# Performance work log

Measured on AMD Instinct MI355X. Metric: run time of the kernel, lower is better.

Reference implementation:

```python
import jax, jax.numpy as jnp
import numpy as np

H = 64   # hidden_dim
E = 5    # num_edge_features
F = 6    # num_node_features
B, W, N = 8, 12, 200
LN_EPS = 1e-5


def _lstm_layer(x, Wih, Whh, bih, bhh):
    # x: [BN, W, Fin] -> full output sequence [BN, W, H] (PyTorch gate order i,f,g,o)
    BN = x.shape[0]
    h0 = jnp.zeros((BN, Whh.shape[1]), x.dtype)
    def step(carry, xt):
        h, c = carry
        g = xt @ Wih.T + h @ Whh.T + (bih + bhh)
        i, f, gg, o = jnp.split(g, 4, axis=-1)
        c = jax.nn.sigmoid(f) * c + jax.nn.sigmoid(i) * jnp.tanh(gg)
        h = jax.nn.sigmoid(o) * jnp.tanh(c)
        return (h, c), h
    _, ys = jax.lax.scan(step, (h0, h0), jnp.swapaxes(x, 0, 1))
    return jnp.swapaxes(ys, 0, 1)


def _layernorm(x, g, b):
    mu = jnp.mean(x, axis=-1, keepdims=True)
    var = jnp.mean(jnp.square(x - mu), axis=-1, keepdims=True)
    return (x - mu) * jax.lax.rsqrt(var + LN_EPS) * g + b


def setup_inputs() -> dict:
    key = jax.random.key(0)
    ks = jax.random.split(key, 32)
    s = 0.05
    d = {
        'node_features': jax.random.normal(ks[0], (B, W, N, F), jnp.float32),
        'edge_features': jax.random.normal(ks[1], (B, W, N, N, E), jnp.float32),
        'adjacency': jax.random.uniform(ks[2], (B, N, N), jnp.float32),
        # LSTM layer 0 (input F) and layer 1 (input H)
        'Wih0': jax.random.normal(ks[3], (4 * H, F), jnp.float32) * s,
        'Whh0': jax.random.normal(ks[4], (4 * H, H), jnp.float32) * s,
        'bih0': jax.random.normal(ks[5], (4 * H,), jnp.float32) * s,
        'bhh0': jax.random.normal(ks[6], (4 * H,), jnp.float32) * s,
        'Wih1': jax.random.normal(ks[7], (4 * H, H), jnp.float32) * s,
        'Whh1': jax.random.normal(ks[8], (4 * H, H), jnp.float32) * s,
        'bih1': jax.random.normal(ks[9], (4 * H,), jnp.float32) * s,
        'bhh1': jax.random.normal(ks[10], (4 * H,), jnp.float32) * s,
        # 2 GCN layers: linear, edge projection, layernorm
        'gcn_W': jax.random.normal(ks[11], (2, H, H), jnp.float32) * s,
        'gcn_b': jax.random.normal(ks[12], (2, H), jnp.float32) * s,
        'ep_W': jax.random.normal(ks[13], (2, H, E), jnp.float32) * s,
        'ep_b': jax.random.normal(ks[14], (2, H), jnp.float32) * s,
        'ln_g': jnp.ones((2, H), jnp.float32),
        'ln_b': jnp.zeros((2, H), jnp.float32),
        # edge MLP: (2H+E) -> H -> H//2 -> 1
        'mlp_W1': jax.random.normal(ks[15], (H, 2 * H + E), jnp.float32) * s,
        'mlp_b1': jax.random.normal(ks[16], (H,), jnp.float32) * s,
        'mlp_W2': jax.random.normal(ks[17], (H // 2, H), jnp.float32) * s,
        'mlp_b2': jax.random.normal(ks[18], (H // 2,), jnp.float32) * s,
        'mlp_W3': jax.random.normal(ks[19], (1, H // 2), jnp.float32) * s,
        'mlp_b3': jax.random.normal(ks[20], (1,), jnp.float32) * s,
    }
    return d


def reference(node_features, edge_features, adjacency,
              Wih0, Whh0, bih0, bhh0, Wih1, Whh1, bih1, bhh1,
              gcn_W, gcn_b, ep_W, ep_b, ln_g, ln_b,
              mlp_W1, mlp_b1, mlp_W2, mlp_b2, mlp_W3, mlp_b3):
    Bn, Wn, Nn, _ = node_features.shape
    # [B,W,N,F] -> [B*N, W, F]
    x = jnp.transpose(node_features, (0, 2, 1, 3)).reshape(Bn * Nn, Wn, -1)
    y0 = _lstm_layer(x, Wih0, Whh0, bih0, bhh0)      # dropout between layers: eval mode (identity)
    y1 = _lstm_layer(y0, Wih1, Whh1, bih1, bhh1)
    h = y1[:, -1, :].reshape(Bn, Nn, H)

    edge_last = edge_features[:, -1]                 # [B,N,N,E]
    for i in range(2):
        edge_h = edge_last @ ep_W[i].T + ep_b[i]     # [B,N,N,H]
        messages = jnp.einsum('bij,bijn->bin', adjacency, edge_h)
        updated = h @ gcn_W[i].T + gcn_b[i] + messages
        h = jax.nn.relu(_layernorm(updated, ln_g[i], ln_b[i]))
        # dropout: eval mode (identity)

    h_i = jnp.broadcast_to(h[:, :, None, :], (Bn, Nn, Nn, H))
    h_j = jnp.broadcast_to(h[:, None, :, :], (Bn, Nn, Nn, H))
    edge_input = jnp.concatenate([h_i, h_j, edge_last], axis=-1)  # [B,N,N,2H+E]
    z = jax.nn.relu(edge_input @ mlp_W1.T + mlp_b1)
    z = jax.nn.relu(z @ mlp_W2.T + mlp_b2)
    logits = (z @ mlp_W3.T + mlp_b3)[..., 0]
    return jax.nn.sigmoid(logits)
```

## Files before the change

kernel.cpp:

```cpp
#include <hip/hip_runtime.h>
#include <math.h>


#define Hd   64
#define Ed   5
#define Fd   6
#define Bd   8
#define Wd   12
#define Nd   200
#define NSEQ (Bd*Nd)
#define NG   (4*Hd)
#define SEQPB 8
#define LNEPS 1e-5f

__device__ __forceinline__ float sigm(float x) { return 1.0f / (1.0f + __expf(-x)); }
__device__ __forceinline__ float tanh_fast(float x) {
  float ax = fabsf(x);
  float t  = __expf(-2.0f * ax);
  float r  = (1.0f - t) / (1.0f + t);
  return copysignf(r, x);
}

__global__ __launch_bounds__(256) void k_prep(
    const float* __restrict__ gcn_W, const float* __restrict__ ep_W,
    const float* __restrict__ W1,
    float* __restrict__ gcnWT, float* __restrict__ epWT,
    float* __restrict__ W1aT, float* __restrict__ W1bT)
{
  int idx = blockIdx.x * 256 + threadIdx.x;
  if (idx < 8192) {
    int round = idx >> 12, rem = idx & 4095;
    int k = rem >> 6, u = rem & 63;
    gcnWT[idx] = gcn_W[round * 4096 + u * 64 + k];
  } else if (idx < 8832) {
    int r0 = idx - 8192;
    int round = r0 / 320, rem = r0 % 320;
    int e = rem >> 6, u = rem & 63;
    epWT[r0] = ep_W[round * 320 + u * Ed + e];
  } else if (idx < 12928) {
    int r0 = idx - 8832;
    int k = r0 >> 6, n = r0 & 63;
    W1aT[r0] = W1[n * 133 + k];
  } else if (idx < 17024) {
    int r0 = idx - 12928;
    int k = r0 >> 6, n = r0 & 63;
    W1bT[r0] = W1[n * 133 + 64 + k];
  }
}

__global__ __launch_bounds__(512, 2) void k_lstm_fused(
    const float* __restrict__ nf,
    const float* __restrict__ Wih0, const float* __restrict__ Whh0,
    const float* __restrict__ bih0, const float* __restrict__ bhh0,
    const float* __restrict__ Wih1, const float* __restrict__ Whh1,
    const float* __restrict__ bih1, const float* __restrict__ bhh1,
    float* __restrict__ hout)
{
  __shared__ float x_sh[SEQPB][Wd * Fd];
  __shared__ float h0_sh[SEQPB][Hd];
  __shared__ float h1_sh[SEQPB][Hd];
  __shared__ float g0_sh[SEQPB][NG];
  __shared__ float g1_sh[SEQPB][NG];

  const int tid  = threadIdx.x;
  const int seq0 = blockIdx.x * SEQPB;
  const int b    = seq0 / Nd;
  const int n0   = seq0 % Nd;

  for (int idx = tid; idx < SEQPB * Wd * Fd; idx += 512) {
    int s = idx / (Wd * Fd), r = idx - s * (Wd * Fd);
    int t = r / Fd, f = r - t * Fd;
    x_sh[s][r] = nf[((b * Wd + t) * Nd + (n0 + s)) * Fd + f];
  }
  ((float*)h0_sh)[tid >= 512 ? 0 : tid] = 0.f;
  ((float*)h1_sh)[tid >= 512 ? 0 : tid] = 0.f;

  const bool isL0 = (tid < 256);
  const int j  = tid & 255;
  const int jt = j >> 6;
  const int u  = tid & 63;
  const int w  = (tid >> 6) & 3;

  float4 wh[16];
  float4 wi1[16];
  float  wx[Fd];
  float  bias;
  if (isL0) {
    const float4* wr = (const float4*)(Whh0 + j * Hd);
    #pragma unroll
    for (int q = 0; q < 16; ++q) wh[q] = wr[q];
    #pragma unroll
    for (int f = 0; f < Fd; ++f) wx[f] = Wih0[j * Fd + f];
    bias = bih0[j] + bhh0[j];
  } else {
    const float4* wr = (const float4*)(Whh1 + j * Hd);
    #pragma unroll
    for (int q = 0; q < 16; ++q) wh[q] = wr[q];
    const float4* xr = (const float4*)(Wih1 + j * Hd);
    #pragma unroll
    for (int q = 0; q < 16; ++q) wi1[q] = xr[q];
    bias = bih1[j] + bhh1[j];
  }

  float cA = 0.f, cB = 0.f;
  float hA = 0.f, hB = 0.f;
  __syncthreads();

  for (int t = 0; t <= Wd; ++t) {
    if (isL0) {
      if (t < Wd) {
        #pragma unroll 2
        for (int s = 0; s < SEQPB; ++s) {
          const float* xp = &x_sh[s][t * Fd];
          float a0 = bias, a1 = 0.f, a2 = 0.f, a3 = 0.f;
          #pragma unroll
          for (int f = 0; f < Fd; ++f) a1 += xp[f] * wx[f];
          const float4* h4 = (const float4*)h0_sh[s];
          #pragma unroll
          for (int q = 0; q < 16; ++q) {
            float4 hv = h4[q];
            float d = hv.x * wh[q].x + hv.y * wh[q].y + hv.z * wh[q].z + hv.w * wh[q].w;
            if ((q & 3) == 0) a0 += d; else if ((q & 3) == 1) a1 += d;
            else if ((q & 3) == 2) a2 += d; else a3 += d;
          }
          float acc = (a0 + a1) + (a2 + a3);
          g0_sh[s][j] = (jt == 2) ? tanh_fast(acc) : sigm(acc);
        }
      }
    } else {
      if (t >= 1) {
        #pragma unroll 2
        for (int s = 0; s < SEQPB; ++s) {
          const float4* y4 = (const float4*)h0_sh[s];
          float xacc = 0.f;
          #pragma unroll
          for (int q = 0; q < 16; ++q) {
            float4 yv = y4[q];
            xacc = fmaf(yv.x, wi1[q].x, xacc);
            xacc = fmaf(yv.y, wi1[q].y, xacc);
            xacc = fmaf(yv.z, wi1[q].z, xacc);
            xacc = fmaf(yv.w, wi1[q].w, xacc);
          }
          xacc += bias;
          float a0 = xacc, a1 = 0.f, a2 = 0.f, a3 = 0.f;
          const float4* h4 = (const float4*)h1_sh[s];
          #pragma unroll
          for (int q = 0; q < 16; ++q) {
            float4 hv = h4[q];
            float d = hv.x * wh[q].x + hv.y * wh[q].y + hv.z * wh[q].z + hv.w * wh[q].w;
            if ((q & 3) == 0) a0 += d; else if ((q & 3) == 1) a1 += d;
            else if ((q & 3) == 2) a2 += d; else a3 += d;
          }
          float acc = (a0 + a1) + (a2 + a3);
          g1_sh[s][j] = (jt == 2) ? tanh_fast(acc) : sigm(acc);
        }
      }
    }
    __syncthreads();

    if (isL0) {
      if (t < Wd) {
        const float* gb = g0_sh[w];
        float iv = gb[u], fv = gb[64 + u], gv = gb[128 + u], ov = gb[192 + u];
        cA = fv * cA + iv * gv;
        hA = ov * tanh_fast(cA);
        h0_sh[w][u] = hA;
        const float* gb2 = g0_sh[w + 4];
        float iv2 = gb2[u], fv2 = gb2[64 + u], gv2 = gb2[128 + u], ov2 = gb2[192 + u];
        cB = fv2 * cB + iv2 * gv2;
        hB = ov2 * tanh_fast(cB);
        h0_sh[w + 4][u] = hB;
      }
    } else {
      if (t >= 1) {
        const float* gb = g1_sh[w];
        float iv = gb[u], fv = gb[64 + u], gv = gb[128 + u], ov = gb[192 + u];
        cA = fv * cA + iv * gv;
        hA = ov * tanh_fast(cA);
        h1_sh[w][u] = hA;
        const float* gb2 = g1_sh[w + 4];
        float iv2 = gb2[u], fv2 = gb2[64 + u], gv2 = gb2[128 + u], ov2 = gb2[192 + u];
        cB = fv2 * cB + iv2 * gv2;
        hB = ov2 * tanh_fast(cB);
        h1_sh[w + 4][u] = hB;
      }
    }
    __syncthreads();
  }

  if (!isL0) {
    hout[(seq0 + w) * Hd + u]     = hA;
    hout[(seq0 + w + 4) * Hd + u] = hB;
  }
}

__global__ __launch_bounds__(256) void k_node(
    const float* __restrict__ ef,    const float* __restrict__ adj,
    const float* __restrict__ h0,
    const float* __restrict__ gcnWT, const float* __restrict__ gcn_b,
    const float* __restrict__ epWT,  const float* __restrict__ ep_b,
    const float* __restrict__ ln_g,  const float* __restrict__ ln_b,
    const float* __restrict__ W1aT,  const float* __restrict__ W1bT,
    const float* __restrict__ b1,
    float* __restrict__ uu, float* __restrict__ vt)
{
  __shared__ float ef_sh[Nd * Ed];
  __shared__ float adj_sh[Nd];
  __shared__ float red[4][6];
  __shared__ float w6[6];
  __shared__ float hcur[Hd];

  const int row = blockIdx.x;
  const int b = row / Nd, i = row % Nd;
  const int tid = threadIdx.x;

  const float* efrow = ef + (size_t)(((b * Wd + (Wd - 1)) * Nd + i)) * (Nd * Ed);
  for (int idx = tid; idx < Nd * Ed; idx += 256) ef_sh[idx] = efrow[idx];
  const float* adjrow = adj + (b * Nd + i) * Nd;
  if (tid < Nd) adj_sh[tid] = adjrow[tid];
  if (tid < Hd) hcur[tid] = h0[row * Hd + tid];
  __syncthreads();

  float p[6] = {0.f, 0.f, 0.f, 0.f, 0.f, 0.f};
  if (tid < Nd) {
    float a = adj_sh[tid];
    p[5] = a;
    #pragma unroll
    for (int k = 0; k < Ed; ++k) p[k] = a * ef_sh[tid * Ed + k];
  }
  #pragma unroll
  for (int k = 0; k < 6; ++k) {
    float v = p[k];
    for (int off = 32; off > 0; off >>= 1) v += __shfl_down(v, off);
    p[k] = v;
  }
  if ((tid & 63) == 0) {
    #pragma unroll
    for (int k = 0; k < 6; ++k) red[tid >> 6][k] = p[k];
  }
  __syncthreads();
  if (tid < 6)
    w6[tid] = red[0][tid] + red[1][tid] + red[2][tid] + red[3][tid];
  __syncthreads();

  const int u = tid & 63;
  #pragma unroll
  for (int round = 0; round < 2; ++round) {
    float hnew = 0.f;
    if (tid < 64) {
      const float* gwT = gcnWT + round * 4096;
      const float* ewT = epWT  + round * 320;
      float acc = gcn_b[round * Hd + u] + w6[5] * ep_b[round * Hd + u];
      #pragma unroll
      for (int e = 0; e < Ed; ++e) acc += w6[e] * ewT[e * 64 + u];
      #pragma unroll 8
      for (int k = 0; k < Hd; ++k) acc += hcur[k] * gwT[k * 64 + u];

      float mu = acc;
      #pragma unroll
      for (int off = 1; off < 64; off <<= 1) mu += __shfl_xor(mu, off);
      mu *= (1.f / 64.f);
      float d = acc - mu;
      float var = d * d;
      #pragma unroll
      for (int off = 1; off < 64; off <<= 1) var += __shfl_xor(var, off);
      var *= (1.f / 64.f);
      float v = d * rsqrtf(var + LNEPS) * ln_g[round * Hd + u] + ln_b[round * Hd + u];
      hnew = fmaxf(v, 0.f);
    }
    __syncthreads();
    if (tid < 64) hcur[tid] = hnew;
    __syncthreads();
  }

  if (tid < 64) {
    float acc = b1[tid];
    #pragma unroll 8
    for (int k = 0; k < Hd; ++k) acc += hcur[k] * W1aT[k * 64 + tid];
    uu[row * Hd + tid] = acc;
  } else if (tid < 128) {
    const int n = tid - 64;
    float acc = 0.f;
    #pragma unroll 8
    for (int k = 0; k < Hd; ++k) acc += hcur[k] * W1bT[k * 64 + n];
    vt[n * NSEQ + row] = acc;
  }
}

__global__ __launch_bounds__(256) void k_mlp(
    const float* __restrict__ ef,
    const float* __restrict__ u, const float* __restrict__ vt,
    const float* __restrict__ W1,
    const float* __restrict__ W2, const float* __restrict__ b2,
    const float* __restrict__ W3, const float* __restrict__ b3,
    float* __restrict__ out)
{
  const int idx = blockIdx.x * 256 + threadIdx.x;
  const int b   = idx / (Nd * Nd);
  const int rem = idx - b * Nd * Nd;
  const int i   = rem / Nd;
  const int jj  = rem - i * Nd;

  const float* e = ef + (((b * Wd + (Wd - 1)) * Nd + i) * Nd + jj) * Ed;
  float e5[Ed];
  #pragma unroll
  for (int q = 0; q < Ed; ++q) e5[q] = e[q];

  const float* ur = u + (b * Nd + i) * Hd;
  const int vcol = b * Nd + jj;

  float z1[64];
  #pragma unroll
  for (int k = 0; k < 64; ++k) {
    float acc = ur[k] + vt[k * NSEQ + vcol];
    const float* w1c = W1 + k * 133 + 128;
    #pragma unroll
    for (int q = 0; q < Ed; ++q) acc += e5[q] * w1c[q];
    z1[k] = fmaxf(acc, 0.f);
  }

  float logit = b3[0];
  #pragma unroll 4
  for (int o = 0; o < 32; ++o) {
    float a0 = b2[o], a1 = 0.f, a2 = 0.f, a3 = 0.f;
    const float* w2 = W2 + o * 64;
    #pragma unroll
    for (int k = 0; k < 64; k += 4) {
      a0 += w2[k]     * z1[k];
      a1 += w2[k + 1] * z1[k + 1];
      a2 += w2[k + 2] * z1[k + 2];
      a3 += w2[k + 3] * z1[k + 3];
    }
    float z2 = fmaxf((a0 + a1) + (a2 + a3), 0.f);
    logit += W3[o] * z2;
  }
  out[idx] = 1.f / (1.f + __expf(-logit));
}

extern "C" void kernel_launch(void* const* d_in, const int* in_sizes, int n_in,
                              void* d_out, int out_size, void* d_ws, size_t ws_size,
                              hipStream_t stream) {
  (void)in_sizes; (void)n_in; (void)out_size; (void)ws_size;
  const float* nf   = (const float*)d_in[0];
  const float* ef   = (const float*)d_in[1];
  const float* adj  = (const float*)d_in[2];
  const float* Wih0 = (const float*)d_in[3];
  const float* Whh0 = (const float*)d_in[4];
  const float* bih0 = (const float*)d_in[5];
  const float* bhh0 = (const float*)d_in[6];
  const float* Wih1 = (const float*)d_in[7];
  const float* Whh1 = (const float*)d_in[8];
  const float* bih1 = (const float*)d_in[9];
  const float* bhh1 = (const float*)d_in[10];
  const float* gcnW = (const float*)d_in[11];
  const float* gcnB = (const float*)d_in[12];
  const float* epW  = (const float*)d_in[13];
  const float* epB  = (const float*)d_in[14];
  const float* lnG  = (const float*)d_in[15];
  const float* lnB  = (const float*)d_in[16];
  const float* W1   = (const float*)d_in[17];
  const float* b1   = (const float*)d_in[18];
  const float* W2   = (const float*)d_in[19];
  const float* b2   = (const float*)d_in[20];
  const float* W3   = (const float*)d_in[21];
  const float* b3   = (const float*)d_in[22];
  float* out = (float*)d_out;

  float* ws   = (float*)d_ws;
  float* h0   = ws;
  float* uu   = h0   + 102400;
  float* vt   = uu   + 102400;
  float* gWT  = vt   + 102400;
  float* eWT  = gWT  + 8192;
  float* W1aT = eWT  + 640;
  float* W1bT = W1aT + 4096;

  k_prep      <<<67,        256, 0, stream>>>(gcnW, epW, W1, gWT, eWT, W1aT, W1bT);
  k_lstm_fused<<<NSEQ/SEQPB,512, 0, stream>>>(nf, Wih0, Whh0, bih0, bhh0,
                                              Wih1, Whh1, bih1, bhh1, h0);
  k_node      <<<1600,      256, 0, stream>>>(ef, adj, h0, gWT, gcnB, eWT, epB,
                                              lnG, lnB, W1aT, W1bT, b1, uu, vt);
  k_mlp       <<<1250,      256, 0, stream>>>(ef, uu, vt, W1, W2, b2, W3, b3, out);
}
```

Before: 266.0 us.

## Keep LSTM hidden state in registers, broadcast via readlane, pipeline layer-1 input projection

Each warp now keeps its hidden and cell state for all 8 sequences in registers, and the h·W products read h values through readlane broadcasts instead of shared memory. The layer-1 input projection moves to the layer-0 half of the block so it runs one step ahead, and the gate buffers are double-buffered, which removes the second __syncthreads per step. The cost is that every warp redundantly computes the state update for all sequences, the per-thread register load grows (wi1 plus wh on the same threads, arrays of 8), and the occupancy hint of 2 blocks per SM is dropped.

```diff
diff --git a/kernel.cpp b/kernel.cpp
--- a/kernel.cpp
+++ b/kernel.cpp
@@ -19,6 +19,9 @@
   float t  = __expf(-2.0f * ax);
   float r  = (1.0f - t) / (1.0f + t);
   return copysignf(r, x);
+}
+__device__ __forceinline__ float rdl(float v, int l) {
+  return __int_as_float(__builtin_amdgcn_readlane(__float_as_int(v), l));
 }
 
 __global__ __launch_bounds__(256) void k_prep(
@@ -48,7 +51,7 @@
   }
 }
 
-__global__ __launch_bounds__(512, 2) void k_lstm_fused(
+__global__ __launch_bounds__(512) void k_lstm_fused(
     const float* __restrict__ nf,
     const float* __restrict__ Wih0, const float* __restrict__ Whh0,
     const float* __restrict__ bih0, const float* __restrict__ bhh0,
@@ -57,10 +60,9 @@
     float* __restrict__ hout)
 {
   __shared__ float x_sh[SEQPB][Wd * Fd];
-  __shared__ float h0_sh[SEQPB][Hd];
-  __shared__ float h1_sh[SEQPB][Hd];
-  __shared__ float g0_sh[SEQPB][NG];
-  __shared__ float g1_sh[SEQPB][NG];
+  __shared__ float g0_sh[2][SEQPB][NG];
+  __shared__ float g1_sh[2][SEQPB][NG];
+  __shared__ float x1_sh[2][SEQPB][NG];
 
   const int tid  = threadIdx.x;
   const int seq0 = blockIdx.x * SEQPB;
@@ -72,125 +74,136 @@
     int t = r / Fd, f = r - t * Fd;
     x_sh[s][r] = nf[((b * Wd + t) * Nd + (n0 + s)) * Fd + f];
   }
-  ((float*)h0_sh)[tid >= 512 ? 0 : tid] = 0.f;
-  ((float*)h1_sh)[tid >= 512 ? 0 : tid] = 0.f;
-
-  const bool isL0 = (tid < 256);
-  const int j  = tid & 255;
-  const int jt = j >> 6;
-  const int u  = tid & 63;
-  const int w  = (tid >> 6) & 3;
+
+  const bool isA = (tid < 256);
+  const int j    = tid & 255;
+  const int jt   = j >> 6;
+  const int lane = tid & 63;
 
   float4 wh[16];
   float4 wi1[16];
   float  wx[Fd];
-  float  bias;
-  if (isL0) {
+  float  bias0 = 0.f, bias1 = 0.f;
+  if (isA) {
     const float4* wr = (const float4*)(Whh0 + j * Hd);
     #pragma unroll
     for (int q = 0; q < 16; ++q) wh[q] = wr[q];
     #pragma unroll
     for (int f = 0; f < Fd; ++f) wx[f] = Wih0[j * Fd + f];
-    bias = bih0[j] + bhh0[j];
+    bias0 = bih0[j] + bhh0[j];
+    const float4* xr = (const float4*)(Wih1 + j * Hd);
+    #pragma unroll
+    for (int q = 0; q < 16; ++q) wi1[q] = xr[q];
+    bias1 = bih1[j] + bhh1[j];
   } else {
     const float4* wr = (const float4*)(Whh1 + j * Hd);
     #pragma unroll
     for (int q = 0; q < 16; ++q) wh[q] = wr[q];
-    const float4* xr = (const float4*)(Wih1 + j * Hd);
-    #pragma unroll
-    for (int q = 0; q < 16; ++q) wi1[q] = xr[q];
-    bias = bih1[j] + bhh1[j];
-  }
-
-  float cA = 0.f, cB = 0.f;
-  float hA = 0.f, hB = 0.f;
+  }
+
+  float hr[SEQPB], cr[SEQPB];
+  #pragma unroll
+  for (int s = 0; s < SEQPB; ++s) { hr[s] = 0.f; cr[s] = 0.f; }
   __syncthreads();
 
-  for (int t = 0; t <= Wd; ++t) {
-    if (isL0) {
+  for (int t = 0; t <= Wd + 1; ++t) {
+    if (isA) {
       if (t < Wd) {
-        #pragma unroll 2
+        #pragma unroll
         for (int s = 0; s < SEQPB; ++s) {
           const float* xp = &x_sh[s][t * Fd];
-          float a0 = bias, a1 = 0.f, a2 = 0.f, a3 = 0.f;
+          float a0 = bias0, a1 = 0.f, a2 = 0.f, a3 = 0.f;
           #pragma unroll
           for (int f = 0; f < Fd; ++f) a1 += xp[f] * wx[f];
-          const float4* h4 = (const float4*)h0_sh[s];
+          float xacc = 0.f;
           #pragma unroll
           for (int q = 0; q < 16; ++q) {
-            float4 hv = h4[q];
-            float d = hv.x * wh[q].x + hv.y * wh[q].y + hv.z * wh[q].z + hv.w * wh[q].w;
+            float hx = rdl(hr[s], 4 * q + 0);
+            float hy = rdl(hr[s], 4 * q + 1);
+            float hz = rdl(hr[s], 4 * q + 2);
+            float hw = rdl(hr[s], 4 * q + 3);
+            float d = hx * wh[q].x + hy * wh[q].y + hz * wh[q].z + hw * wh[q].w;
+            if ((q & 3) == 0) a0 += d; else if ((q & 3) == 1) a1 += d;
+            else if ((q & 3) == 2) a2 += d; else a3 += d;
+            xacc = fmaf(hx, wi1[q].x, xacc);
+            xacc = fmaf(hy, wi1[q].y, xacc);
+            xacc = fmaf(hz, wi1[q].z, xacc);
+            xacc = fmaf(hw, wi1[q].w, xacc);
+          }
+          float acc = (a0 + a1) + (a2 + a3);
+          g0_sh[t & 1][s][j] = (jt == 2) ? tanh_fast(acc) : sigm(acc);
+          if (t >= 1) x1_sh[t & 1][s][j] = xacc + bias1;
+        }
+      } else if (t == Wd) {
+        #pragma unroll
+        for (int s = 0; s < SEQPB; ++s) {
+          float xacc = 0.f;
+          #pragma unroll
+          for (int q = 0; q < 16; ++q) {
+            float hx = rdl(hr[s], 4 * q + 0);
+            float hy = rdl(hr[s], 4 * q + 1);
+            float hz = rdl(hr[s], 4 * q + 2);
+            float hw = rdl(hr[s], 4 * q + 3);
+            xacc = fmaf(hx, wi1[q].x, xacc);
+            xacc = fmaf(hy, wi1[q].y, xacc);
+            xacc = fmaf(hz, wi1[q].z, xacc);
+            xacc = fmaf(hw, wi1[q].w, xacc);
+          }
+          x1_sh[t & 1][s][j] = xacc + bias1;
+        }
+      }
+    } else {
+      if (t >= 2) {
+        #pragma unroll
+        for (int s = 0; s < SEQPB; ++s) {
+          float a0 = x1_sh[(t - 1) & 1][s][j];
+          float a1 = 0.f, a2 = 0.f, a3 = 0.f;
+          #pragma unroll
+          for (int q = 0; q < 16; ++q) {
+            float hx = rdl(hr[s], 4 * q + 0);
+            float hy = rdl(hr[s], 4 * q + 1);
+            float hz = rdl(hr[s], 4 * q + 2);
+            float hw = rdl(hr[s], 4 * q + 3);
+            float d = hx * wh[q].x + hy * wh[q].y + hz * wh[q].z + hw * wh[q].w;
             if ((q & 3) == 0) a0 += d; else if ((q & 3) == 1) a1 += d;
             else if ((q & 3) == 2) a2 += d; else a3 += d;
           }
           float acc = (a0 + a1) + (a2 + a3);
-          g0_sh[s][j] = (jt == 2) ? tanh_fast(acc) : sigm(acc);
-        }
-      }
-    } else {
-      if (t >= 1) {
-        #pragma unroll 2
-        for (int s = 0; s < SEQPB; ++s) {
-          const float4* y4 = (const float4*)h0_sh[s];
-          float xacc = 0.f;
-          #pragma unroll
-          for (int q = 0; q < 16; ++q) {
-            float4 yv = y4[q];
-            xacc = fmaf(yv.x, wi1[q].x, xacc);
-            xacc = fmaf(yv.y, wi1[q].y, xacc);
-            xacc = fmaf(yv.z, wi1[q].z, xacc);
-            xacc = fmaf(yv.w, wi1[q].w, xacc);
-          }
-          xacc += bias;
-          float a0 = xacc, a1 = 0.f, a2 = 0.f, a3 = 0.f;
-          const float4* h4 = (const float4*)h1_sh[s];
-          #pragma unroll
-          for (int q = 0; q < 16; ++q) {
-            float4 hv = h4[q];
-            float d = hv.x * wh[q].x + hv.y * wh[q].y + hv.z * wh[q].z + hv.w * wh[q].w;
-            if ((q & 3) == 0) a0 += d; else if ((q & 3) == 1) a1 += d;
-            else if ((q & 3) == 2) a2 += d; else a3 += d;
-          }
-          float acc = (a0 + a1) + (a2 + a3);
-          g1_sh[s][j] = (jt == 2) ? tanh_fast(acc) : sigm(acc);
+          g1_sh[t & 1][s][j] = (jt == 2) ? tanh_fast(acc) : sigm(acc);
         }
       }
     }
     __syncthreads();
 
-    if (isL0) {
+    if (isA) {
       if (t < Wd) {
-        const float* gb = g0_sh[w];
-        float iv = gb[u], fv = gb[64 + u], gv = gb[128 + u], ov = gb[192 + u];
-        cA = fv * cA + iv * gv;
-        hA = ov * tanh_fast(cA);
-        h0_sh[w][u] = hA;
-        const float* gb2 = g0_sh[w + 4];
-        float iv2 = gb2[u], fv2 = gb2[64 + u], gv2 = gb2[128 + u], ov2 = gb2[192 + u];
-        cB = fv2 * cB + iv2 * gv2;
-        hB = ov2 * tanh_fast(cB);
-        h0_sh[w + 4][u] = hB;
+        #pragma unroll
+        for (int s = 0; s < SEQPB; ++s) {
+          const float* gb = g0_sh[t & 1][s];
+          float iv = gb[lane], fv = gb[64 + lane];
+          float gv = gb[128 + lane], ov = gb[192 + lane];
+          cr[s] = fv * cr[s] + iv * gv;
+          hr[s] = ov * tanh_fast(cr[s]);
+        }
       }
     } else {
-      if (t >= 1) {
-        const float* gb = g1_sh[w];
-        float iv = gb[u], fv = gb[64 + u], gv = gb[128 + u], ov = gb[192 + u];
-        cA = fv * cA + iv * gv;
-        hA = ov * tanh_fast(cA);
-        h1_sh[w][u] = hA;
-        const float* gb2 = g1_sh[w + 4];
-        float iv2 = gb2[u], fv2 = gb2[64 + u], gv2 = gb2[128 + u], ov2 = gb2[192 + u];
-        cB = fv2 * cB + iv2 * gv2;
-        hB = ov2 * tanh_fast(cB);
-        h1_sh[w + 4][u] = hB;
+      if (t >= 2) {
+        #pragma unroll
+        for (int s = 0; s < SEQPB; ++s) {
+          const float* gb = g1_sh[t & 1][s];
+          float iv = gb[lane], fv = gb[64 + lane];
+          float gv = gb[128 + lane], ov = gb[192 + lane];
+          cr[s] = fv * cr[s] + iv * gv;
+          hr[s] = ov * tanh_fast(cr[s]);
+        }
       }
     }
-    __syncthreads();
-  }
-
-  if (!isL0) {
-    hout[(seq0 + w) * Hd + u]     = hA;
-    hout[(seq0 + w + 4) * Hd + u] = hB;
+  }
+
+  if (tid >= 256 && tid < 320) {
+    #pragma unroll
+    for (int s = 0; s < SEQPB; ++s)
+      hout[(seq0 + s) * Hd + lane] = hr[s];
   }
 }
 
```

New measurement: 275.4 us. 1.04x slower.

## Rebalance LSTM layer work, use readlane GCN in node kernel, batch MLP loads

Applied to the files above, without the earlier changes.

The layer-1 input projection (Wih1·h0) moves to the layer-0 threads, which compute it alongside their recurrent dot product and pass it through a double-buffered shared array, so the layer-1 half only does its own recurrence. This adds one pipeline step. The node kernel keeps the hidden vector in registers, broadcasts it with readlane instead of shared memory, and drops two barriers. The MLP kernel groups its u/vt loads in blocks of eight to expose memory-level parallelism. Layer-0 threads now hold more registers, which risks spills at 512 threads per block.

```diff
diff --git a/kernel.cpp b/kernel.cpp
--- a/kernel.cpp
+++ b/kernel.cpp
@@ -19,6 +19,9 @@
   float t  = __expf(-2.0f * ax);
   float r  = (1.0f - t) / (1.0f + t);
   return copysignf(r, x);
+}
+__device__ __forceinline__ float rdl(float v, int l) {
+  return __int_as_float(__builtin_amdgcn_readlane(__float_as_int(v), l));
 }
 
 __global__ __launch_bounds__(256) void k_prep(
@@ -61,6 +64,7 @@
   __shared__ float h1_sh[SEQPB][Hd];
   __shared__ float g0_sh[SEQPB][NG];
   __shared__ float g1_sh[SEQPB][NG];
+  __shared__ float x1_sh[2][SEQPB][NG];
 
   const int tid  = threadIdx.x;
   const int seq0 = blockIdx.x * SEQPB;
@@ -72,10 +76,10 @@
     int t = r / Fd, f = r - t * Fd;
     x_sh[s][r] = nf[((b * Wd + t) * Nd + (n0 + s)) * Fd + f];
   }
-  ((float*)h0_sh)[tid >= 512 ? 0 : tid] = 0.f;
-  ((float*)h1_sh)[tid >= 512 ? 0 : tid] = 0.f;
-
-  const bool isL0 = (tid < 256);
+  ((float*)h0_sh)[tid] = 0.f;
+  ((float*)h1_sh)[tid] = 0.f;
+
+  const bool isA = (tid < 256);
   const int j  = tid & 255;
   const int jt = j >> 6;
   const int u  = tid & 63;
@@ -84,37 +88,38 @@
   float4 wh[16];
   float4 wi1[16];
   float  wx[Fd];
-  float  bias;
-  if (isL0) {
+  float  bias0 = 0.f, bias1 = 0.f;
+  if (isA) {
     const float4* wr = (const float4*)(Whh0 + j * Hd);
     #pragma unroll
     for (int q = 0; q < 16; ++q) wh[q] = wr[q];
     #pragma unroll
     for (int f = 0; f < Fd; ++f) wx[f] = Wih0[j * Fd + f];
-    bias = bih0[j] + bhh0[j];
+    bias0 = bih0[j] + bhh0[j];
+    const float4* xr = (const float4*)(Wih1 + j * Hd);
+    #pragma unroll
+    for (int q = 0; q < 16; ++q) wi1[q] = xr[q];
+    bias1 = bih1[j] + bhh1[j];
   } else {
     const float4* wr = (const float4*)(Whh1 + j * Hd);
     #pragma unroll
     for (int q = 0; q < 16; ++q) wh[q] = wr[q];
-    const float4* xr = (const float4*)(Wih1 + j * Hd);
-    #pragma unroll
-    for (int q = 0; q < 16; ++q) wi1[q] = xr[q];
-    bias = bih1[j] + bhh1[j];
   }
 
   float cA = 0.f, cB = 0.f;
   float hA = 0.f, hB = 0.f;
   __syncthreads();
 
-  for (int t = 0; t <= Wd; ++t) {
-    if (isL0) {
+  for (int t = 0; t <= Wd + 1; ++t) {
+    if (isA) {
       if (t < Wd) {
         #pragma unroll 2
         for (int s = 0; s < SEQPB; ++s) {
           const float* xp = &x_sh[s][t * Fd];
-          float a0 = bias, a1 = 0.f, a2 = 0.f, a3 = 0.f;
+          float a0 = bias0, a1 = 0.f, a2 = 0.f, a3 = 0.f;
           #pragma unroll
           for (int f = 0; f < Fd; ++f) a1 += xp[f] * wx[f];
+          float xacc = 0.f;
           const float4* h4 = (const float4*)h0_sh[s];
           #pragma unroll
           for (int q = 0; q < 16; ++q) {
@@ -122,27 +127,37 @@
             float d = hv.x * wh[q].x + hv.y * wh[q].y + hv.z * wh[q].z + hv.w * wh[q].w;
             if ((q & 3) == 0) a0 += d; else if ((q & 3) == 1) a1 += d;
             else if ((q & 3) == 2) a2 += d; else a3 += d;
+            xacc = fmaf(hv.x, wi1[q].x, xacc);
+            xacc = fmaf(hv.y, wi1[q].y, xacc);
+            xacc = fmaf(hv.z, wi1[q].z, xacc);
+            xacc = fmaf(hv.w, wi1[q].w, xacc);
           }
           float acc = (a0 + a1) + (a2 + a3);
           g0_sh[s][j] = (jt == 2) ? tanh_fast(acc) : sigm(acc);
+          if (t >= 1) x1_sh[t & 1][s][j] = xacc + bias1;
+        }
+      } else if (t == Wd) {
+        #pragma unroll 2
+        for (int s = 0; s < SEQPB; ++s) {
+          float xacc = 0.f;
+          const float4* h4 = (const float4*)h0_sh[s];
+          #pragma unroll
+          for (int q = 0; q < 16; ++q) {
+            float4 hv = h4[q];
+            xacc = fmaf(hv.x, wi1[q].x, xacc);
+            xacc = fmaf(hv.y, wi1[q].y, xacc);
+            xacc = fmaf(hv.z, wi1[q].z, xacc);
+            xacc = fmaf(hv.w, wi1[q].w, xacc);
+          }
+          x1_sh[t & 1][s][j] = xacc + bias1;
         }
       }
     } else {
-      if (t >= 1) {
+      if (t >= 2) {
         #pragma unroll 2
         for (int s = 0; s < SEQPB; ++s) {
-          const float4* y4 = (const float4*)h0_sh[s];
-          float xacc = 0.f;
-          #pragma unroll
-          for (int q = 0; q < 16; ++q) {
-            float4 yv = y4[q];
-            xacc = fmaf(yv.x, wi1[q].x, xacc);
-            xacc = fmaf(yv.y, wi1[q].y, xacc);
-            xacc = fmaf(yv.z, wi1[q].z, xacc);
-            xacc = fmaf(yv.w, wi1[q].w, xacc);
-          }
-          xacc += bias;
-          float a0 = xacc, a1 = 0.f, a2 = 0.f, a3 = 0.f;
+          float a0 = x1_sh[(t - 1) & 1][s][j];
+          float a1 = 0.f, a2 = 0.f, a3 = 0.f;
           const float4* h4 = (const float4*)h1_sh[s];
           #pragma unroll
           for (int q = 0; q < 16; ++q) {
@@ -158,7 +173,7 @@
     }
     __syncthreads();
 
-    if (isL0) {
+    if (isA) {
       if (t < Wd) {
         const float* gb = g0_sh[w];
         float iv = gb[u], fv = gb[64 + u], gv = gb[128 + u], ov = gb[192 + u];
@@ -172,7 +187,7 @@
         h0_sh[w + 4][u] = hB;
       }
     } else {
-      if (t >= 1) {
+      if (t >= 2) {
         const float* gb = g1_sh[w];
         float iv = gb[u], fv = gb[64 + u], gv = gb[128 + u], ov = gb[192 + u];
         cA = fv * cA + iv * gv;
@@ -188,7 +203,7 @@
     __syncthreads();
   }
 
-  if (!isL0) {
+  if (!isA) {
     hout[(seq0 + w) * Hd + u]     = hA;
     hout[(seq0 + w + 4) * Hd + u] = hB;
   }
@@ -207,18 +222,18 @@
   __shared__ float ef_sh[Nd * Ed];
   __shared__ float adj_sh[Nd];
   __shared__ float red[4][6];
-  __shared__ float w6[6];
-  __shared__ float hcur[Hd];
 
   const int row = blockIdx.x;
   const int b = row / Nd, i = row % Nd;
   const int tid = threadIdx.x;
+  const int lane = tid & 63;
+  const int wv = tid >> 6;
 
   const float* efrow = ef + (size_t)(((b * Wd + (Wd - 1)) * Nd + i)) * (Nd * Ed);
   for (int idx = tid; idx < Nd * Ed; idx += 256) ef_sh[idx] = efrow[idx];
   const float* adjrow = adj + (b * Nd + i) * Nd;
   if (tid < Nd) adj_sh[tid] = adjrow[tid];
-  if (tid < Hd) hcur[tid] = h0[row * Hd + tid];
+  float hreg = h0[row * Hd + lane];
   __syncthreads();
 
   float p[6] = {0.f, 0.f, 0.f, 0.f, 0.f, 0.f};
@@ -234,56 +249,52 @@
     for (int off = 32; off > 0; off >>= 1) v += __shfl_down(v, off);
     p[k] = v;
   }
-  if ((tid & 63) == 0) {
-    #pragma unroll
-    for (int k = 0; k < 6; ++k) red[tid >> 6][k] = p[k];
+  if (lane == 0) {
+    #pragma unroll
+    for (int k = 0; k < 6; ++k) red[wv][k] = p[k];
   }
   __syncthreads();
-  if (tid < 6)
-    w6[tid] = red[0][tid] + red[1][tid] + red[2][tid] + red[3][tid];
-  __syncthreads();
-
-  const int u = tid & 63;
+
+  if (wv >= 2) return;
+
+  float w6r[6];
+  #pragma unroll
+  for (int k = 0; k < 6; ++k)
+    w6r[k] = red[0][k] + red[1][k] + red[2][k] + red[3][k];
+
   #pragma unroll
   for (int round = 0; round < 2; ++round) {
-    float hnew = 0.f;
-    if (tid < 64) {
-      const float* gwT = gcnWT + round * 4096;
-      const float* ewT = epWT  + round * 320;
-      float acc = gcn_b[round * Hd + u] + w6[5] * ep_b[round * Hd + u];
-      #pragma unroll
-      for (int e = 0; e < Ed; ++e) acc += w6[e] * ewT[e * 64 + u];
-      #pragma unroll 8
-      for (int k = 0; k < Hd; ++k) acc += hcur[k] * gwT[k * 64 + u];
-
-      float mu = acc;
-      #pragma unroll
-      for (int off = 1; off < 64; off <<= 1) mu += __shfl_xor(mu, off);
-      mu *= (1.f / 64.f);
-      float d = acc - mu;
-      float var = d * d;
-      #pragma unroll
-      for (int off = 1; off < 64; off <<= 1) var += __shfl_xor(var, off);
-      var *= (1.f / 64.f);
-      float v = d * rsqrtf(var + LNEPS) * ln_g[round * Hd + u] + ln_b[round * Hd + u];
-      hnew = fmaxf(v, 0.f);
-    }
-    __syncthreads();
-    if (tid < 64) hcur[tid] = hnew;
-    __syncthreads();
-  }
-
-  if (tid < 64) {
-    float acc = b1[tid];
-    #pragma unroll 8
-    for (int k = 0; k < Hd; ++k) acc += hcur[k] * W1aT[k * 64 + tid];
-    uu[row * Hd + tid] = acc;
-  } else if (tid < 128) {
-    const int n = tid - 64;
+    const float* gwT = gcnWT + round * 4096;
+    const float* ewT = epWT  + round * 320;
+    float acc = gcn_b[round * Hd + lane] + w6r[5] * ep_b[round * Hd + lane];
+    #pragma unroll
+    for (int e = 0; e < Ed; ++e) acc += w6r[e] * ewT[e * 64 + lane];
+    #pragma unroll
+    for (int k = 0; k < Hd; ++k) acc += rdl(hreg, k) * gwT[k * 64 + lane];
+
+    float mu = acc;
+    #pragma unroll
+    for (int off = 1; off < 64; off <<= 1) mu += __shfl_xor(mu, off);
+    mu *= (1.f / 64.f);
+    float d = acc - mu;
+    float var = d * d;
+    #pragma unroll
+    for (int off = 1; off < 64; off <<= 1) var += __shfl_xor(var, off);
+    var *= (1.f / 64.f);
+    float v = d * rsqrtf(var + LNEPS) * ln_g[round * Hd + lane] + ln_b[round * Hd + lane];
+    hreg = fmaxf(v, 0.f);
+  }
+
+  if (wv == 0) {
+    float acc = b1[lane];
+    #pragma unroll
+    for (int k = 0; k < Hd; ++k) acc += rdl(hreg, k) * W1aT[k * 64 + lane];
+    uu[row * Hd + lane] = acc;
+  } else {
     float acc = 0.f;
-    #pragma unroll 8
-    for (int k = 0; k < Hd; ++k) acc += hcur[k] * W1bT[k * 64 + n];
-    vt[n * NSEQ + row] = acc;
+    #pragma unroll
+    for (int k = 0; k < Hd; ++k) acc += rdl(hreg, k) * W1bT[k * 64 + lane];
+    vt[lane * NSEQ + row] = acc;
   }
 }
 
@@ -311,12 +322,22 @@
 
   float z1[64];
   #pragma unroll
-  for (int k = 0; k < 64; ++k) {
-    float acc = ur[k] + vt[k * NSEQ + vcol];
-    const float* w1c = W1 + k * 133 + 128;
-    #pragma unroll
-    for (int q = 0; q < Ed; ++q) acc += e5[q] * w1c[q];
-    z1[k] = fmaxf(acc, 0.f);
+  for (int kb = 0; kb < 8; ++kb) {
+    float uvv[8], vvv[8];
+    #pragma unroll
+    for (int q = 0; q < 8; ++q) {
+      uvv[q] = ur[kb * 8 + q];
+      vvv[q] = vt[(kb * 8 + q) * NSEQ + vcol];
+    }
+    #pragma unroll
+    for (int q = 0; q < 8; ++q) {
+      int k = kb * 8 + q;
+      float acc = uvv[q] + vvv[q];
+      const float* w1c = W1 + k * 133 + 128;
+      #pragma unroll
+      for (int qq = 0; qq < Ed; ++qq) acc += e5[qq] * w1c[qq];
+      z1[k] = fmaxf(acc, 0.f);
+    }
   }
 
   float logit = b3[0];
```

New measurement: 379.5 us. 1.43x slower.

## Split LSTM layer-1 input projection from recurrence into pipelined thread roles

Applied to the files above, without the earlier changes.

The fused two-layer LSTM kernel gives layer 1's input projection (Wih1·h0) to one 128-thread group and its recurrent projection (Whh1·h1) to another. Each thread now computes two gate rows, and the input projection is staged through a double-buffered shared array, so the recurrence consumes it one step later and the pipeline gains a step. This shortens the critical path of the layer-1 threads, which previously did both dot products per gate. In exchange, register use per thread rises (two 64-float weight rows kept in registers), and launch bounds drop to one block per SIMD set, which reduces occupancy.

```diff
diff --git a/kernel.cpp b/kernel.cpp
--- a/kernel.cpp
+++ b/kernel.cpp
@@ -48,7 +48,7 @@
   }
 }
 
-__global__ __launch_bounds__(512, 2) void k_lstm_fused(
+__global__ __launch_bounds__(512, 1) void k_lstm_fused(
     const float* __restrict__ nf,
     const float* __restrict__ Wih0, const float* __restrict__ Whh0,
     const float* __restrict__ bih0, const float* __restrict__ bhh0,
@@ -61,6 +61,7 @@
   __shared__ float h1_sh[SEQPB][Hd];
   __shared__ float g0_sh[SEQPB][NG];
   __shared__ float g1_sh[SEQPB][NG];
+  __shared__ float x1_sh[2][SEQPB][NG];
 
   const int tid  = threadIdx.x;
   const int seq0 = blockIdx.x * SEQPB;
@@ -72,47 +73,52 @@
     int t = r / Fd, f = r - t * Fd;
     x_sh[s][r] = nf[((b * Wd + t) * Nd + (n0 + s)) * Fd + f];
   }
-  ((float*)h0_sh)[tid >= 512 ? 0 : tid] = 0.f;
-  ((float*)h1_sh)[tid >= 512 ? 0 : tid] = 0.f;
-
-  const bool isL0 = (tid < 256);
-  const int j  = tid & 255;
-  const int jt = j >> 6;
-  const int u  = tid & 63;
-  const int w  = (tid >> 6) & 3;
-
-  float4 wh[16];
-  float4 wi1[16];
-  float  wx[Fd];
-  float  bias;
-  if (isL0) {
+  ((float*)h0_sh)[tid] = 0.f;
+  ((float*)h1_sh)[tid] = 0.f;
+
+  const int role = tid >> 7;
+  const int u    = tid & 63;
+  const int w    = (tid >> 6) & 3;
+
+  float4 wh[16];  float wx[Fd];  float bias0 = 0.f;
+  float4 wiA[16], wiB[16];  float biasA = 0.f, biasB = 0.f;
+  float4 whA[16], whB[16];
+  const int jsub = tid & 127;
+
+  if (role < 2) {
+    const int j = tid;
     const float4* wr = (const float4*)(Whh0 + j * Hd);
     #pragma unroll
     for (int q = 0; q < 16; ++q) wh[q] = wr[q];
     #pragma unroll
     for (int f = 0; f < Fd; ++f) wx[f] = Wih0[j * Fd + f];
-    bias = bih0[j] + bhh0[j];
+    bias0 = bih0[j] + bhh0[j];
+  } else if (role == 2) {
+    const float4* ra = (const float4*)(Wih1 + jsub * Hd);
+    const float4* rb = (const float4*)(Wih1 + (jsub + 128) * Hd);
+    #pragma unroll
+    for (int q = 0; q < 16; ++q) { wiA[q] = ra[q]; wiB[q] = rb[q]; }
+    biasA = bih1[jsub] + bhh1[jsub];
+    biasB = bih1[jsub + 128] + bhh1[jsub + 128];
   } else {
-    const float4* wr = (const float4*)(Whh1 + j * Hd);
-    #pragma unroll
-    for (int q = 0; q < 16; ++q) wh[q] = wr[q];
-    const float4* xr = (const float4*)(Wih1 + j * Hd);
-    #pragma unroll
-    for (int q = 0; q < 16; ++q) wi1[q] = xr[q];
-    bias = bih1[j] + bhh1[j];
+    const float4* ra = (const float4*)(Whh1 + jsub * Hd);
+    const float4* rb = (const float4*)(Whh1 + (jsub + 128) * Hd);
+    #pragma unroll
+    for (int q = 0; q < 16; ++q) { whA[q] = ra[q]; whB[q] = rb[q]; }
   }
 
   float cA = 0.f, cB = 0.f;
   float hA = 0.f, hB = 0.f;
   __syncthreads();
 
-  for (int t = 0; t <= Wd; ++t) {
-    if (isL0) {
+  for (int t = 0; t <= Wd + 1; ++t) {
+    if (role < 2) {
       if (t < Wd) {
+        const int j = tid, jt = j >> 6;
         #pragma unroll 2
         for (int s = 0; s < SEQPB; ++s) {
           const float* xp = &x_sh[s][t * Fd];
-          float a0 = bias, a1 = 0.f, a2 = 0.f, a3 = 0.f;
+          float a0 = bias0, a1 = 0.f, a2 = 0.f, a3 = 0.f;
           #pragma unroll
           for (int f = 0; f < Fd; ++f) a1 += xp[f] * wx[f];
           const float4* h4 = (const float4*)h0_sh[s];
@@ -127,38 +133,58 @@
           g0_sh[s][j] = (jt == 2) ? tanh_fast(acc) : sigm(acc);
         }
       }
-    } else {
-      if (t >= 1) {
+    } else if (role == 2) {
+      if (t >= 1 && t <= Wd) {
         #pragma unroll 2
         for (int s = 0; s < SEQPB; ++s) {
-          const float4* y4 = (const float4*)h0_sh[s];
-          float xacc = 0.f;
+          const float4* h4 = (const float4*)h0_sh[s];
+          float xa = 0.f, xb = 0.f;
           #pragma unroll
           for (int q = 0; q < 16; ++q) {
-            float4 yv = y4[q];
-            xacc = fmaf(yv.x, wi1[q].x, xacc);
-            xacc = fmaf(yv.y, wi1[q].y, xacc);
-            xacc = fmaf(yv.z, wi1[q].z, xacc);
-            xacc = fmaf(yv.w, wi1[q].w, xacc);
+            float4 hv = h4[q];
+            xa = fmaf(hv.x, wiA[q].x, xa);
+            xa = fmaf(hv.y, wiA[q].y, xa);
+            xa = fmaf(hv.z, wiA[q].z, xa);
+            xa = fmaf(hv.w, wiA[q].w, xa);
+            xb = fmaf(hv.x, wiB[q].x, xb);
+            xb = fmaf(hv.y, wiB[q].y, xb);
+            xb = fmaf(hv.z, wiB[q].z, xb);
+            xb = fmaf(hv.w, wiB[q].w, xb);
           }
-          xacc += bias;
-          float a0 = xacc, a1 = 0.f, a2 = 0.f, a3 = 0.f;
+          x1_sh[t & 1][s][jsub]       = xa + biasA;
+          x1_sh[t & 1][s][jsub + 128] = xb + biasB;
+        }
+      }
+    } else {
+      if (t >= 2) {
+        const int jtA = jsub >> 6;
+        const int jtB = 2 + (jsub >> 6);
+        #pragma unroll 2
+        for (int s = 0; s < SEQPB; ++s) {
+          const float* xv = x1_sh[(t - 1) & 1][s];
+          float a0 = xv[jsub],       a1 = 0.f, a2 = 0.f, a3 = 0.f;
+          float e0 = xv[jsub + 128], e1 = 0.f, e2 = 0.f, e3 = 0.f;
           const float4* h4 = (const float4*)h1_sh[s];
           #pragma unroll
           for (int q = 0; q < 16; ++q) {
             float4 hv = h4[q];
-            float d = hv.x * wh[q].x + hv.y * wh[q].y + hv.z * wh[q].z + hv.w * wh[q].w;
-            if ((q & 3) == 0) a0 += d; else if ((q & 3) == 1) a1 += d;
-            else if ((q & 3) == 2) a2 += d; else a3 += d;
+            float dA = hv.x * whA[q].x + hv.y * whA[q].y + hv.z * whA[q].z + hv.w * whA[q].w;
+            float dB = hv.x * whB[q].x + hv.y * whB[q].y + hv.z * whB[q].z + hv.w * whB[q].w;
+            if ((q & 3) == 0) { a0 += dA; e0 += dB; }
+            else if ((q & 3) == 1) { a1 += dA; e1 += dB; }
+            else if ((q & 3) == 2) { a2 += dA; e2 += dB; }
+            else { a3 += dA; e3 += dB; }
           }
-          float acc = (a0 + a1) + (a2 + a3);
-          g1_sh[s][j] = (jt == 2) ? tanh_fast(acc) : sigm(acc);
+          float accA = (a0 + a1) + (a2 + a3);
+          float accB = (e0 + e1) + (e2 + e3);
+          g1_sh[s][jsub]       = (jtA == 2) ? tanh_fast(accA) : sigm(accA);
+          g1_sh[s][jsub + 128] = (jtB == 2) ? tanh_fast(accB) : sigm(accB);
         }
       }
     }
     __syncthreads();
 
-    if (isL0) {
+    if (tid < 256) {
       if (t < Wd) {
         const float* gb = g0_sh[w];
         float iv = gb[u], fv = gb[64 + u], gv = gb[128 + u], ov = gb[192 + u];
@@ -172,7 +198,7 @@
         h0_sh[w + 4][u] = hB;
       }
     } else {
-      if (t >= 1) {
+      if (t >= 2) {
         const float* gb = g1_sh[w];
         float iv = gb[u], fv = gb[64 + u], gv = gb[128 + u], ov = gb[192 + u];
         cA = fv * cA + iv * gv;
@@ -188,7 +214,7 @@
     __syncthreads();
   }
 
-  if (!isL0) {
+  if (tid >= 256) {
     hout[(seq0 + w) * Hd + u]     = hA;
     hout[(seq0 + w + 4) * Hd + u] = hB;
   }
```

After: 778.6 us. 2.93x slower.
